# Performance work log

Hardware: AMD Instinct MI355X
Metric: run time of the kernel (lower is better)

The kernel has to match this reference:

```python
import jax, jax.numpy as jnp
import numpy as np


def setup_inputs() -> dict:
    key = jax.random.key(0)
    k1, k2, k3 = jax.random.split(key, 3)
    B, L, D = 2, 8192, 1024
    x = jax.random.normal(k1, (B, L, D), dtype=jnp.float32)
    h = jax.random.normal(k2, (L, D), dtype=jnp.float32)
    bias = jax.random.normal(k3, (D,), dtype=jnp.float32) * 0.02
    return {"x": x, "h": h, "bias": bias}


def reference(x, h, bias):
    # x: (B, L, D), h: (filter_len, D), bias: (D,)
    B, L, D = x.shape
    filter_len = h.shape[0]
    # next power of two >= L + filter_len - 1 (static, from shapes)
    fft_size = 1 << int(L + filter_len - 1).bit_length()
    x_f = jnp.fft.rfft(x, n=fft_size, axis=1)          # (B, fft_size//2+1, D) complex
    h_f = jnp.fft.rfft(h, n=fft_size, axis=0)          # (fft_size//2+1, D) complex
    y = jnp.fft.irfft(x_f * h_f[None, :, :], n=fft_size, axis=1)
    y = y[:, :L, :]                                    # causal-length truncation
    return y + bias
```

## Files before the change

### kernel.cpp

```cpp
#include <hip/hip_runtime.h>

#define D_CH   1024
#define L_SEQ  8192
#define NCH    32
#define W_N    3.8349519697141029e-4f
#define W128A  4.90873852123405e-2f

__device__ __forceinline__ float bf2f(unsigned v){
  union { float f; unsigned u; } x; x.u = v << 16;
  return x.f;
}
__device__ __forceinline__ unsigned packc(float r, float i){
  unsigned u;
  asm("v_cvt_pk_bf16_f32 %0, %1, %2" : "=v"(u) : "v"(r), "v"(i));
  return u;
}
__device__ __forceinline__ float2 upk(unsigned u){
  return make_float2(bf2f(u & 0xffffu), bf2f(u >> 16));
}
__device__ __forceinline__ float4 upk2(uint2 u){
  return make_float4(bf2f(u.x & 0xffffu), bf2f(u.x >> 16),
                     bf2f(u.y & 0xffffu), bf2f(u.y >> 16));
}
__device__ __forceinline__ float4 cmul2(float4 a, float cs, float sn){
  return make_float4(a.x*cs - a.y*sn, a.x*sn + a.y*cs,
                     a.z*cs - a.w*sn, a.z*sn + a.w*cs);
}

__device__ __host__ constexpr int bitrev4(int j){
  return ((j&1)<<3)|((j&2)<<1)|((j&4)>>1)|((j&8)>>3);
}
__device__ __host__ constexpr int bitrev3(int j){
  return ((j&1)<<2)|(j&2)|((j&4)>>2);
}

template<int SGN>
__device__ __forceinline__ void dft16(float2* x){
  const float TC[8] = {1.f, 0.9238795325f, 0.7071067812f, 0.3826834324f,
                       0.f, -0.3826834324f, -0.7071067812f, -0.9238795325f};
  const float TS[8] = {0.f, -0.3826834324f, -0.7071067812f, -0.9238795325f,
                       -1.f, -0.9238795325f, -0.7071067812f, -0.3826834324f};
#pragma unroll
  for (int len = 16; len >= 2; len >>= 1){
    const int half = len >> 1, tstep = 16 / len;
#pragma unroll
    for (int st = 0; st < 16; st += len){
#pragma unroll
      for (int j = 0; j < half; j++){
        const float wr = TC[j*tstep];
        const float wi = (SGN > 0) ? TS[j*tstep] : -TS[j*tstep];
        const int a = st + j, b = a + half;
        const float ur = x[a].x, ui = x[a].y;
        const float vr = x[b].x, vi = x[b].y;
        x[a].x = ur + vr; x[a].y = ui + vi;
        const float dr = ur - vr, di = ui - vi;
        x[b].x = dr*wr - di*wi;
        x[b].y = dr*wi + di*wr;
      }
    }
  }
}

template<int SGN>
__device__ __forceinline__ void dft8(float2* x){
  const float TC[4] = {1.f, 0.7071067812f, 0.f, -0.7071067812f};
  const float TS[4] = {0.f, -0.7071067812f, -1.f, -0.7071067812f};
#pragma unroll
  for (int len = 8; len >= 2; len >>= 1){
    const int half = len >> 1, tstep = 8 / len;
#pragma unroll
    for (int st = 0; st < 8; st += len){
#pragma unroll
      for (int j = 0; j < half; j++){
        const float wr = TC[j*tstep];
        const float wi = (SGN > 0) ? TS[j*tstep] : -TS[j*tstep];
        const int a = st + j, b = a + half;
        const float ur = x[a].x, ui = x[a].y;
        const float vr = x[b].x, vi = x[b].y;
        x[a].x = ur + vr; x[a].y = ui + vi;
        const float dr = ur - vr, di = ui - vi;
        x[b].x = dr*wr - di*wi;
        x[b].y = dr*wi + di*wr;
      }
    }
  }
}

template<int SGN>
__device__ __forceinline__ void dft16v4(float4* x){
  const float TC[8] = {1.f, 0.9238795325f, 0.7071067812f, 0.3826834324f,
                       0.f, -0.3826834324f, -0.7071067812f, -0.9238795325f};
  const float TS[8] = {0.f, -0.3826834324f, -0.7071067812f, -0.9238795325f,
                       -1.f, -0.9238795325f, -0.7071067812f, -0.3826834324f};
#pragma unroll
  for (int len = 16; len >= 2; len >>= 1){
    const int half = len >> 1, tstep = 16 / len;
#pragma unroll
    for (int st = 0; st < 16; st += len){
#pragma unroll
      for (int j = 0; j < half; j++){
        const float wr = TC[j*tstep];
        const float wi = (SGN > 0) ? TS[j*tstep] : -TS[j*tstep];
        const int a = st + j, b = a + half;
        const float4 u = x[a], v = x[b];
        x[a] = make_float4(u.x+v.x, u.y+v.y, u.z+v.z, u.w+v.w);
        const float4 dd = make_float4(u.x-v.x, u.y-v.y, u.z-v.z, u.w-v.w);
        x[b] = make_float4(dd.x*wr - dd.y*wi, dd.x*wi + dd.y*wr,
                           dd.z*wr - dd.w*wi, dd.z*wi + dd.w*wr);
      }
    }
  }
}

template<int SGN>
__device__ __forceinline__ void dft8v4(float4* x){
  const float TC[4] = {1.f, 0.7071067812f, 0.f, -0.7071067812f};
  const float TS[4] = {0.f, -0.7071067812f, -1.f, -0.7071067812f};
#pragma unroll
  for (int len = 8; len >= 2; len >>= 1){
    const int half = len >> 1, tstep = 8 / len;
#pragma unroll
    for (int st = 0; st < 8; st += len){
#pragma unroll
      for (int j = 0; j < half; j++){
        const float wr = TC[j*tstep];
        const float wi = (SGN > 0) ? TS[j*tstep] : -TS[j*tstep];
        const int a = st + j, b = a + half;
        const float4 u = x[a], v = x[b];
        x[a] = make_float4(u.x+v.x, u.y+v.y, u.z+v.z, u.w+v.w);
        const float4 dd = make_float4(u.x-v.x, u.y-v.y, u.z-v.z, u.w-v.w);
        x[b] = make_float4(dd.x*wr - dd.y*wi, dd.x*wi + dd.y*wr,
                           dd.z*wr - dd.w*wi, dd.z*wi + dd.w*wr);
      }
    }
  }
}

__device__ __forceinline__ void build_twF(float2* twF, int tid){
  if (tid < 128){
    const int pp = tid >> 4, kk = tid & 15;
    float sn, cs;
    __sincosf(-W128A * (float)(pp * kk), &sn, &cs);
    twF[tid] = make_float2(cs, sn);
  }
}

template<int SGN>
__device__ __forceinline__ void fft128(float2* v, float2* lds,
                                       const float2* twF, int ch, int p){
  dft16<SGN>(v);
#pragma unroll
  for (int slot = 0; slot < 8; slot++){
    const int r = bitrev3(slot);
    const float2 t = twF[p*16 + 2*r];
    const float cs = t.x;
    const float sn = (SGN > 0) ? t.y : -t.y;
    const float2 a = v[slot];
    lds[(p*8 + r)*NCH + ch] = make_float2(a.x*cs - a.y*sn, a.x*sn + a.y*cs);
  }
  __syncthreads();
  float2 t8[8];
#pragma unroll
  for (int pp = 0; pp < 8; pp++) t8[pp] = lds[(pp*8 + p)*NCH + ch];
  dft8<SGN>(t8);
#pragma unroll
  for (int t = 0; t < 8; t++) v[t] = t8[t];
  __syncthreads();
#pragma unroll
  for (int slot = 8; slot < 16; slot++){
    const int r = bitrev3(slot - 8);
    const float2 t = twF[p*16 + 2*r + 1];
    const float cs = t.x;
    const float sn = (SGN > 0) ? t.y : -t.y;
    const float2 a = v[slot];
    lds[(p*8 + r)*NCH + ch] = make_float2(a.x*cs - a.y*sn, a.x*sn + a.y*cs);
  }
  __syncthreads();
#pragma unroll
  for (int pp = 0; pp < 8; pp++) t8[pp] = lds[(pp*8 + p)*NCH + ch];
  dft8<SGN>(t8);
#pragma unroll
  for (int t = 0; t < 8; t++) v[8 + t] = t8[t];
}

template<int SGN>
__device__ __forceinline__ void fft128v4(float4* v, float4* lds4,
                                         const float2* twF, int ch, int p){
  dft16v4<SGN>(v);
#pragma unroll
  for (int slot = 0; slot < 8; slot++){
    const int r = bitrev3(slot);
    const float2 t = twF[p*16 + 2*r];
    const float cs = t.x;
    const float sn = (SGN > 0) ? t.y : -t.y;
    lds4[(p*8 + r)*32 + ch] = cmul2(v[slot], cs, sn);
  }
  __syncthreads();
  float4 t8[8];
#pragma unroll
  for (int pp = 0; pp < 8; pp++) t8[pp] = lds4[(pp*8 + p)*32 + ch];
  dft8v4<SGN>(t8);
#pragma unroll
  for (int t = 0; t < 8; t++) v[t] = t8[t];
  __syncthreads();
#pragma unroll
  for (int slot = 8; slot < 16; slot++){
    const int r = bitrev3(slot - 8);
    const float2 t = twF[p*16 + 2*r + 1];
    const float cs = t.x;
    const float sn = (SGN > 0) ? t.y : -t.y;
    lds4[(p*8 + r)*32 + ch] = cmul2(v[slot], cs, sn);
  }
  __syncthreads();
#pragma unroll
  for (int pp = 0; pp < 8; pp++) t8[pp] = lds4[(pp*8 + p)*32 + ch];
  dft8v4<SGN>(t8);
#pragma unroll
  for (int t = 0; t < 8; t++) v[8 + t] = t8[t];
}

__global__ __launch_bounds__(256, 4)
void k1_step1(const float* __restrict__ x, const float* __restrict__ h,
              unsigned* __restrict__ Az, unsigned* __restrict__ Ah){
  __shared__ float4 lds4[64*32];
  __shared__ float2 twF[128];
  __shared__ float2 twO[128];
  const int n2 = blockIdx.x, dg = blockIdx.y, mode = blockIdx.z;
  const int tid = threadIdx.x;
  const int ch = tid & 31, p = tid >> 5;
  const int d = dg*64 + 2*ch;

  build_twF(twF, tid);
  if (tid >= 128 && tid < 256){
    const int k1v = tid - 128;
    float sn, cs;
    __sincosf(-W_N * (float)(k1v * n2), &sn, &cs);
    twO[k1v] = make_float2(cs, sn);
  }

  float4 v[16];
  if (mode == 0){
    const float* x0 = x;
    const float* x1 = x + (size_t)L_SEQ * D_CH;
#pragma unroll
    for (int q = 0; q < 8; q++){
      const size_t off = (size_t)(n2 + 128*(p + 8*q)) * D_CH + d;
      const float2 a = *(const float2*)(x0 + off);
      const float2 b = *(const float2*)(x1 + off);
      v[q] = make_float4(a.x, b.x, a.y, b.y);
    }
  } else {
#pragma unroll
    for (int q = 0; q < 8; q++){
      const size_t off = (size_t)(n2 + 128*(p + 8*q)) * D_CH + d;
      const float2 a = *(const float2*)(h + off);
      v[q] = make_float4(a.x, 0.f, a.y, 0.f);
    }
  }
#pragma unroll
  for (int q = 8; q < 16; q++) v[q] = make_float4(0.f, 0.f, 0.f, 0.f);

  __syncthreads();
  fft128v4<1>(v, lds4, twF, ch, p);

  unsigned* __restrict__ A = mode ? Ah : Az;
#pragma unroll
  for (int c = 0; c < 2; c++){
#pragma unroll
    for (int t = 0; t < 8; t++){
      const int k1v = (2*p + c) + 16*bitrev3(t);
      const float2 w = twO[k1v];
      const float4 r = cmul2(v[c*8 + t], w.x, w.y);
      *(uint2*)&A[((size_t)k1v*128 + n2)*D_CH + d] =
        make_uint2(packc(r.x, r.y), packc(r.z, r.w));
    }
  }
}

__global__ __launch_bounds__(256, 4)
void k2_zh(unsigned* __restrict__ Az, const unsigned* __restrict__ Ah){
  __shared__ float2 lds[64*NCH];
  __shared__ float2 twF[128];
  const int k1 = blockIdx.x, dg = blockIdx.y;
  const int tid = threadIdx.x;
  const int ch = tid & (NCH-1), p = tid >> 5;
  const int d = dg*NCH + ch;
  const size_t base = (size_t)k1 * 128 * D_CH + d;

  build_twF(twF, tid);

  unsigned ha[16], za[16];
#pragma unroll
  for (int q = 0; q < 16; q++)
    ha[q] = Ah[base + (size_t)(p + 8*q) * D_CH];
#pragma unroll
  for (int q = 0; q < 16; q++)
    za[q] = Az[base + (size_t)(p + 8*q) * D_CH];

  __syncthreads();

  float2 v[16];
#pragma unroll
  for (int q = 0; q < 16; q++) v[q] = upk(ha[q]);
  fft128<1>(v, lds, twF, ch, p);
  unsigned hs[16];
  const float sc = 1.0f / 16384.0f;
#pragma unroll
  for (int i = 0; i < 16; i++) hs[i] = packc(v[i].x * sc, v[i].y * sc);
  __syncthreads();

#pragma unroll
  for (int q = 0; q < 16; q++) v[q] = upk(za[q]);
  fft128<1>(v, lds, twF, ch, p);

#pragma unroll
  for (int i = 0; i < 16; i++){
    const float2 hv = upk(hs[i]);
    const float zr = v[i].x, zi = v[i].y;
    v[i] = make_float2(zr*hv.x - zi*hv.y, zr*hv.y + zi*hv.x);
  }

  __syncthreads();
  float2 w[8];
#pragma unroll
  for (int c = 0; c < 2; c++)
#pragma unroll
    for (int t = 0; t < 8; t += 2){
      const int k2 = (2*p + c) + 16*bitrev3(t);
      lds[k2*NCH + ch] = v[c*8 + t];
    }
  __syncthreads();
#pragma unroll
  for (int q = 0; q < 8; q++) w[q] = lds[(p + 8*q)*NCH + ch];
  __syncthreads();
#pragma unroll
  for (int c = 0; c < 2; c++)
#pragma unroll
    for (int t = 1; t < 8; t += 2){
      const int k2 = (2*p + c) + 16*bitrev3(t) - 64;
      lds[k2*NCH + ch] = v[c*8 + t];
    }
  __syncthreads();
#pragma unroll
  for (int q = 0; q < 8; q++) v[8 + q] = lds[(p + 8*q)*NCH + ch];
  __syncthreads();
#pragma unroll
  for (int q = 0; q < 8; q++) v[q] = w[q];

  fft128<-1>(v, lds, twF, ch, p);

#pragma unroll
  for (int c = 0; c < 2; c++){
#pragma unroll
    for (int t = 0; t < 8; t++){
      const int m2 = (2*p + c) + 16*bitrev3(t);
      const float2 a = v[c*8 + t];
      Az[base + (size_t)m2 * D_CH] = packc(a.x, a.y);
    }
  }
}

__global__ __launch_bounds__(256, 4)
void k3_inv2(const unsigned* __restrict__ Bz, const float* __restrict__ bias,
             float* __restrict__ out){
  __shared__ float4 lds4[64*32];
  __shared__ float2 twF[128];
  __shared__ float2 twI[128];
  const int m2 = blockIdx.x, dg = blockIdx.y;
  const int tid = threadIdx.x;
  const int ch = tid & 31, p = tid >> 5;
  const int d = dg*64 + 2*ch;
  const float2 bv = *(const float2*)(bias + d);

  build_twF(twF, tid);
  if (tid >= 128 && tid < 256){
    const int k1 = tid - 128;
    float sn, cs;
    __sincosf(W_N * (float)(m2 * k1), &sn, &cs);
    twI[k1] = make_float2(cs, sn);
  }

  uint2 raw[16];
#pragma unroll
  for (int q = 0; q < 16; q++){
    const int k1 = p + 8*q;
    raw[q] = *(const uint2*)&Bz[((size_t)k1*128 + m2) * D_CH + d];
  }

  __syncthreads();

  float4 v[16];
#pragma unroll
  for (int q = 0; q < 16; q++){
    const float2 w = twI[p + 8*q];
    v[q] = cmul2(upk2(raw[q]), w.x, w.y);
  }

  fft128v4<-1>(v, lds4, twF, ch, p);

#pragma unroll
  for (int c = 0; c < 2; c++){
#pragma unroll
    for (int t = 0; t < 8; t += 2){
      const int m1 = (2*p + c) + 16*bitrev3(t);
      const int tseq = m2 + 128*m1;
      const float4 a = v[c*8 + t];
      *(float2*)&out[(size_t)tseq * D_CH + d] =
        make_float2(a.x + bv.x, a.z + bv.y);
      *(float2*)&out[(size_t)(L_SEQ + tseq) * D_CH + d] =
        make_float2(a.y + bv.x, a.w + bv.y);
    }
  }
}

extern "C" void kernel_launch(void* const* d_in, const int* in_sizes, int n_in,
                              void* d_out, int out_size, void* d_ws, size_t ws_size,
                              hipStream_t stream){
  (void)in_sizes; (void)n_in; (void)out_size;
  const float* x    = (const float*)d_in[0];
  const float* h    = (const float*)d_in[1];
  const float* bias = (const float*)d_in[2];
  float* out = (float*)d_out;

  const size_t REGION = (size_t)128 * 128 * D_CH * sizeof(unsigned);
  unsigned *r1, *r2;
  if (ws_size >= 2 * REGION){
    r1 = (unsigned*)d_ws;
    r2 = (unsigned*)((char*)d_ws + REGION);
  } else {
    r1 = (unsigned*)d_out;
    r2 = (unsigned*)d_ws;
  }

  const dim3 blk(256, 1, 1);
  hipLaunchKernelGGL(k1_step1, dim3(128,16,2), blk, 0, stream, x, h, r1, r2);
  hipLaunchKernelGGL(k2_zh,    dim3(128,32,1), blk, 0, stream, r1, r2);
  hipLaunchKernelGGL(k3_inv2,  dim3(128,16,1), blk, 0, stream, r1, bias, out);
}
```

Baseline: 236.7 us.

## Make FFT stages wave-local with double-buffered register prefetch across tiles

Result: slower. 388.9 us (+64.3%).

```diff
diff --git a/kernel.cpp b/kernel.cpp
--- a/kernel.cpp
+++ b/kernel.cpp
@@ -2,7 +2,6 @@
 
 #define D_CH   1024
 #define L_SEQ  8192
-#define NCH    32
 #define W_N    3.8349519697141029e-4f
 #define W128A  4.90873852123405e-2f
 
@@ -27,11 +26,13 @@
                      a.z*cs - a.w*sn, a.z*sn + a.w*cs);
 }
 
-__device__ __host__ constexpr int bitrev4(int j){
-  return ((j&1)<<3)|((j&2)<<1)|((j&4)>>1)|((j&8)>>3);
-}
 __device__ __host__ constexpr int bitrev3(int j){
   return ((j&1)<<2)|(j&2)|((j&4)>>2);
+}
+
+__device__ __forceinline__ void lds_fence(){
+  asm volatile("s_waitcnt lgkmcnt(0)" ::: "memory");
+  __builtin_amdgcn_sched_barrier(0);
 }
 
 template<int SGN>
@@ -113,14 +114,24 @@
 }
 
 template<int SGN>
-__device__ __forceinline__ void dft8v4(float4* x){
-  const float TC[4] = {1.f, 0.7071067812f, 0.f, -0.7071067812f};
-  const float TS[4] = {0.f, -0.7071067812f, -1.f, -0.7071067812f};
+__device__ __forceinline__ void dft16zv4(float4* x){
+  const float TC[8] = {1.f, 0.9238795325f, 0.7071067812f, 0.3826834324f,
+                       0.f, -0.3826834324f, -0.7071067812f, -0.9238795325f};
+  const float TS[8] = {0.f, -0.3826834324f, -0.7071067812f, -0.9238795325f,
+                       -1.f, -0.9238795325f, -0.7071067812f, -0.3826834324f};
+#pragma unroll
+  for (int j = 0; j < 8; j++){
+    const float wr = TC[j];
+    const float wi = (SGN > 0) ? TS[j] : -TS[j];
+    const float4 u = x[j];
+    x[j+8] = make_float4(u.x*wr - u.y*wi, u.x*wi + u.y*wr,
+                         u.z*wr - u.w*wi, u.z*wi + u.w*wr);
+  }
 #pragma unroll
   for (int len = 8; len >= 2; len >>= 1){
-    const int half = len >> 1, tstep = 8 / len;
-#pragma unroll
-    for (int st = 0; st < 8; st += len){
+    const int half = len >> 1, tstep = 16 / len;
+#pragma unroll
+    for (int st = 0; st < 16; st += len){
 #pragma unroll
       for (int j = 0; j < half; j++){
         const float wr = TC[j*tstep];
@@ -136,279 +147,361 @@
   }
 }
 
-__device__ __forceinline__ void build_twF(float2* twF, int tid){
+template<int SGN>
+__device__ __forceinline__ void dft8v4(float4* x){
+  const float TC[4] = {1.f, 0.7071067812f, 0.f, -0.7071067812f};
+  const float TS[4] = {0.f, -0.7071067812f, -1.f, -0.7071067812f};
+#pragma unroll
+  for (int len = 8; len >= 2; len >>= 1){
+    const int half = len >> 1, tstep = 8 / len;
+#pragma unroll
+    for (int st = 0; st < 8; st += len){
+#pragma unroll
+      for (int j = 0; j < half; j++){
+        const float wr = TC[j*tstep];
+        const float wi = (SGN > 0) ? TS[j*tstep] : -TS[j*tstep];
+        const int a = st + j, b = a + half;
+        const float4 u = x[a], v = x[b];
+        x[a] = make_float4(u.x+v.x, u.y+v.y, u.z+v.z, u.w+v.w);
+        const float4 dd = make_float4(u.x-v.x, u.y-v.y, u.z-v.z, u.w-v.w);
+        x[b] = make_float4(dd.x*wr - dd.y*wi, dd.x*wi + dd.y*wr,
+                           dd.z*wr - dd.w*wi, dd.z*wi + dd.w*wr);
+      }
+    }
+  }
+}
+
+template<int SGN, bool ZT>
+__device__ __forceinline__ void fft128w4(float4* v, float4* buf,
+                                         const float2* twF, int c8, int p){
+  lds_fence();
+  if (ZT) dft16zv4<SGN>(v); else dft16v4<SGN>(v);
+#pragma unroll
+  for (int slot = 0; slot < 8; slot++){
+    const int r = bitrev3(slot);
+    const float2 t = twF[p*16 + 2*r];
+    const float cs = t.x, sn = (SGN > 0) ? t.y : -t.y;
+    buf[(p*8 + r)*8 + c8] = cmul2(v[slot], cs, sn);
+  }
+  lds_fence();
+  float4 t8[8];
+#pragma unroll
+  for (int pp = 0; pp < 8; pp++) t8[pp] = buf[(pp*8 + p)*8 + c8];
+  lds_fence();
+  dft8v4<SGN>(t8);
+#pragma unroll
+  for (int t = 0; t < 8; t++) v[t] = t8[t];
+#pragma unroll
+  for (int slot = 8; slot < 16; slot++){
+    const int r = bitrev3(slot - 8);
+    const float2 t = twF[p*16 + 2*r + 1];
+    const float cs = t.x, sn = (SGN > 0) ? t.y : -t.y;
+    buf[(p*8 + r)*8 + c8] = cmul2(v[slot], cs, sn);
+  }
+  lds_fence();
+#pragma unroll
+  for (int pp = 0; pp < 8; pp++) t8[pp] = buf[(pp*8 + p)*8 + c8];
+  dft8v4<SGN>(t8);
+#pragma unroll
+  for (int t = 0; t < 8; t++) v[8 + t] = t8[t];
+}
+
+template<int SGN>
+__device__ __forceinline__ void fft128w2(float2* v, float2* buf,
+                                         const float2* twF, int c8, int p){
+  lds_fence();
+  dft16<SGN>(v);
+#pragma unroll
+  for (int slot = 0; slot < 8; slot++){
+    const int r = bitrev3(slot);
+    const float2 t = twF[p*16 + 2*r];
+    const float cs = t.x, sn = (SGN > 0) ? t.y : -t.y;
+    const float2 a = v[slot];
+    buf[(p*8 + r)*9 + c8] = make_float2(a.x*cs - a.y*sn, a.x*sn + a.y*cs);
+  }
+  lds_fence();
+  float2 t8[8];
+#pragma unroll
+  for (int pp = 0; pp < 8; pp++) t8[pp] = buf[(pp*8 + p)*9 + c8];
+  lds_fence();
+  dft8<SGN>(t8);
+#pragma unroll
+  for (int t = 0; t < 8; t++) v[t] = t8[t];
+#pragma unroll
+  for (int slot = 8; slot < 16; slot++){
+    const int r = bitrev3(slot - 8);
+    const float2 t = twF[p*16 + 2*r + 1];
+    const float cs = t.x, sn = (SGN > 0) ? t.y : -t.y;
+    const float2 a = v[slot];
+    buf[(p*8 + r)*9 + c8] = make_float2(a.x*cs - a.y*sn, a.x*sn + a.y*cs);
+  }
+  lds_fence();
+#pragma unroll
+  for (int pp = 0; pp < 8; pp++) t8[pp] = buf[(pp*8 + p)*9 + c8];
+  dft8<SGN>(t8);
+#pragma unroll
+  for (int t = 0; t < 8; t++) v[8 + t] = t8[t];
+}
+
+__global__ __launch_bounds__(256, 2)
+void k1_step1(const float* __restrict__ x, const float* __restrict__ h,
+              unsigned* __restrict__ Az, unsigned* __restrict__ Ah){
+  __shared__ float4 xch[4][64*8];
+  __shared__ float2 twF[128];
+  __shared__ float2 twO[128];
+  const int n2 = blockIdx.x, dh = blockIdx.y, mode = blockIdx.z;
+  const int tid = threadIdx.x;
+  const int wv = tid >> 6, lane = tid & 63;
+  const int p = lane >> 3, c8 = lane & 7;
+  const float* x1 = x + (size_t)L_SEQ * D_CH;
+  unsigned* __restrict__ A = mode ? Ah : Az;
+  float4* buf = xch[wv];
+
+  float2 a0[8], a1[8], b0[8], b1[8];
+
+  auto loadT = [&](int i, float2 (&r0)[8], float2 (&r1)[8]){
+    const int d = dh*512 + i*64 + wv*16 + c8*2;
+    if (mode == 0){
+#pragma unroll
+      for (int q = 0; q < 8; q++){
+        const size_t off = (size_t)(n2 + 128*(p + 8*q)) * D_CH + d;
+        r0[q] = *(const float2*)(x  + off);
+        r1[q] = *(const float2*)(x1 + off);
+      }
+    } else {
+#pragma unroll
+      for (int q = 0; q < 8; q++){
+        const size_t off = (size_t)(n2 + 128*(p + 8*q)) * D_CH + d;
+        r0[q] = *(const float2*)(h + off);
+      }
+    }
+  };
+
+  auto runT = [&](int i, float2 (&r0)[8], float2 (&r1)[8]){
+    const int d = dh*512 + i*64 + wv*16 + c8*2;
+    float4 v[16];
+    if (mode == 0){
+#pragma unroll
+      for (int q = 0; q < 8; q++)
+        v[q] = make_float4(r0[q].x, r1[q].x, r0[q].y, r1[q].y);
+    } else {
+#pragma unroll
+      for (int q = 0; q < 8; q++)
+        v[q] = make_float4(r0[q].x, 0.f, r0[q].y, 0.f);
+    }
+    fft128w4<1, true>(v, buf, twF, c8, p);
+#pragma unroll
+    for (int c = 0; c < 2; c++)
+#pragma unroll
+      for (int t = 0; t < 8; t++){
+        const int k1v = (2*p + c) + 16*bitrev3(t);
+        if (mode == 1 && k1v > 64) continue;
+        const float2 w = twO[k1v];
+        const float4 r = cmul2(v[c*8 + t], w.x, w.y);
+        *(uint2*)&A[((size_t)k1v*128 + n2)*D_CH + d] =
+          make_uint2(packc(r.x, r.y), packc(r.z, r.w));
+      }
+  };
+
+  loadT(0, a0, a1);
   if (tid < 128){
     const int pp = tid >> 4, kk = tid & 15;
     float sn, cs;
     __sincosf(-W128A * (float)(pp * kk), &sn, &cs);
     twF[tid] = make_float2(cs, sn);
-  }
-}
-
-template<int SGN>
-__device__ __forceinline__ void fft128(float2* v, float2* lds,
-                                       const float2* twF, int ch, int p){
-  dft16<SGN>(v);
-#pragma unroll
-  for (int slot = 0; slot < 8; slot++){
-    const int r = bitrev3(slot);
-    const float2 t = twF[p*16 + 2*r];
-    const float cs = t.x;
-    const float sn = (SGN > 0) ? t.y : -t.y;
-    const float2 a = v[slot];
-    lds[(p*8 + r)*NCH + ch] = make_float2(a.x*cs - a.y*sn, a.x*sn + a.y*cs);
-  }
-  __syncthreads();
-  float2 t8[8];
-#pragma unroll
-  for (int pp = 0; pp < 8; pp++) t8[pp] = lds[(pp*8 + p)*NCH + ch];
-  dft8<SGN>(t8);
-#pragma unroll
-  for (int t = 0; t < 8; t++) v[t] = t8[t];
-  __syncthreads();
-#pragma unroll
-  for (int slot = 8; slot < 16; slot++){
-    const int r = bitrev3(slot - 8);
-    const float2 t = twF[p*16 + 2*r + 1];
-    const float cs = t.x;
-    const float sn = (SGN > 0) ? t.y : -t.y;
-    const float2 a = v[slot];
-    lds[(p*8 + r)*NCH + ch] = make_float2(a.x*cs - a.y*sn, a.x*sn + a.y*cs);
-  }
-  __syncthreads();
-#pragma unroll
-  for (int pp = 0; pp < 8; pp++) t8[pp] = lds[(pp*8 + p)*NCH + ch];
-  dft8<SGN>(t8);
-#pragma unroll
-  for (int t = 0; t < 8; t++) v[8 + t] = t8[t];
-}
-
-template<int SGN>
-__device__ __forceinline__ void fft128v4(float4* v, float4* lds4,
-                                         const float2* twF, int ch, int p){
-  dft16v4<SGN>(v);
-#pragma unroll
-  for (int slot = 0; slot < 8; slot++){
-    const int r = bitrev3(slot);
-    const float2 t = twF[p*16 + 2*r];
-    const float cs = t.x;
-    const float sn = (SGN > 0) ? t.y : -t.y;
-    lds4[(p*8 + r)*32 + ch] = cmul2(v[slot], cs, sn);
-  }
-  __syncthreads();
-  float4 t8[8];
-#pragma unroll
-  for (int pp = 0; pp < 8; pp++) t8[pp] = lds4[(pp*8 + p)*32 + ch];
-  dft8v4<SGN>(t8);
-#pragma unroll
-  for (int t = 0; t < 8; t++) v[t] = t8[t];
-  __syncthreads();
-#pragma unroll
-  for (int slot = 8; slot < 16; slot++){
-    const int r = bitrev3(slot - 8);
-    const float2 t = twF[p*16 + 2*r + 1];
-    const float cs = t.x;
-    const float sn = (SGN > 0) ? t.y : -t.y;
-    lds4[(p*8 + r)*32 + ch] = cmul2(v[slot], cs, sn);
-  }
-  __syncthreads();
-#pragma unroll
-  for (int pp = 0; pp < 8; pp++) t8[pp] = lds4[(pp*8 + p)*32 + ch];
-  dft8v4<SGN>(t8);
-#pragma unroll
-  for (int t = 0; t < 8; t++) v[8 + t] = t8[t];
-}
-
-__global__ __launch_bounds__(256, 4)
-void k1_step1(const float* __restrict__ x, const float* __restrict__ h,
-              unsigned* __restrict__ Az, unsigned* __restrict__ Ah){
-  __shared__ float4 lds4[64*32];
-  __shared__ float2 twF[128];
-  __shared__ float2 twO[128];
-  const int n2 = blockIdx.x, dg = blockIdx.y, mode = blockIdx.z;
-  const int tid = threadIdx.x;
-  const int ch = tid & 31, p = tid >> 5;
-  const int d = dg*64 + 2*ch;
-
-  build_twF(twF, tid);
-  if (tid >= 128 && tid < 256){
+  } else {
     const int k1v = tid - 128;
     float sn, cs;
     __sincosf(-W_N * (float)(k1v * n2), &sn, &cs);
     twO[k1v] = make_float2(cs, sn);
   }
-
-  float4 v[16];
-  if (mode == 0){
-    const float* x0 = x;
-    const float* x1 = x + (size_t)L_SEQ * D_CH;
-#pragma unroll
-    for (int q = 0; q < 8; q++){
-      const size_t off = (size_t)(n2 + 128*(p + 8*q)) * D_CH + d;
-      const float2 a = *(const float2*)(x0 + off);
-      const float2 b = *(const float2*)(x1 + off);
-      v[q] = make_float4(a.x, b.x, a.y, b.y);
-    }
+  __syncthreads();
+
+#pragma unroll
+  for (int i = 0; i < 8; i++){
+    if (i & 1){
+      if (i+1 < 8) loadT(i+1, a0, a1);
+      runT(i, b0, b1);
+    } else {
+      if (i+1 < 8) loadT(i+1, b0, b1);
+      runT(i, a0, a1);
+    }
+  }
+}
+
+__global__ __launch_bounds__(256, 2)
+void k2_zh(unsigned* __restrict__ Az, const unsigned* __restrict__ Ah){
+  __shared__ float2 rbuf[4][128*9];
+  __shared__ float2 twF[128];
+  __shared__ float2 tw1[128];
+  const int k1 = blockIdx.x, dq = blockIdx.y;
+  const int tid = threadIdx.x;
+  const int wv = tid >> 6, lane = tid & 63;
+  const int p = lane >> 3, c8 = lane & 7;
+  const int k1r = (k1 > 64) ? 128 - k1 : k1;
+  float2* buf = rbuf[wv];
+
+  unsigned haA[16], zaA[16], haB[16], zaB[16];
+
+  auto loadT = [&](int i, unsigned (&ha)[16], unsigned (&za)[16]){
+    const int d = dq*256 + i*32 + wv*8 + c8;
+    const size_t bh = (size_t)k1r * 128 * D_CH + d;
+    const size_t bz = (size_t)k1  * 128 * D_CH + d;
+#pragma unroll
+    for (int q = 0; q < 16; q++) ha[q] = Ah[bh + (size_t)(p + 8*q) * D_CH];
+#pragma unroll
+    for (int q = 0; q < 16; q++) za[q] = Az[bz + (size_t)(p + 8*q) * D_CH];
+  };
+
+  auto runT = [&](int i, unsigned (&ha)[16], unsigned (&za)[16]){
+    const int d = dq*256 + i*32 + wv*8 + c8;
+    const size_t bz = (size_t)k1 * 128 * D_CH + d;
+    float2 v[16];
+    if (k1 <= 64){
+#pragma unroll
+      for (int q = 0; q < 16; q++) v[q] = upk(ha[q]);
+    } else {
+#pragma unroll
+      for (int q = 0; q < 16; q++){
+        const float2 a = upk(ha[q]);
+        const float2 t = tw1[p + 8*q];
+        v[q] = make_float2(t.x*a.x + t.y*a.y, t.y*a.x - t.x*a.y);
+      }
+    }
+    fft128w2<1>(v, buf, twF, c8, p);
+    unsigned hs[16];
+    const float sc = 1.0f / 16384.0f;
+#pragma unroll
+    for (int j = 0; j < 16; j++) hs[j] = packc(v[j].x * sc, v[j].y * sc);
+
+#pragma unroll
+    for (int q = 0; q < 16; q++) v[q] = upk(za[q]);
+    fft128w2<1>(v, buf, twF, c8, p);
+
+#pragma unroll
+    for (int j = 0; j < 16; j++){
+      const float2 hv = upk(hs[j]);
+      const float zr = v[j].x, zi = v[j].y;
+      v[j] = make_float2(zr*hv.x - zi*hv.y, zr*hv.y + zi*hv.x);
+    }
+
+    lds_fence();
+#pragma unroll
+    for (int c = 0; c < 2; c++)
+#pragma unroll
+      for (int t = 0; t < 8; t++){
+        const int k2i = (2*p + c) + 16*bitrev3(t);
+        buf[k2i*9 + c8] = v[c*8 + t];
+      }
+    lds_fence();
+#pragma unroll
+    for (int q = 0; q < 16; q++) v[q] = buf[(p + 8*q)*9 + c8];
+
+    fft128w2<-1>(v, buf, twF, c8, p);
+
+#pragma unroll
+    for (int c = 0; c < 2; c++)
+#pragma unroll
+      for (int t = 0; t < 8; t++){
+        const int m2 = (2*p + c) + 16*bitrev3(t);
+        const float2 a = v[c*8 + t];
+        Az[bz + (size_t)m2 * D_CH] = packc(a.x, a.y);
+      }
+  };
+
+  loadT(0, haA, zaA);
+  if (tid < 128){
+    const int pp = tid >> 4, kk = tid & 15;
+    float sn, cs;
+    __sincosf(-W128A * (float)(pp * kk), &sn, &cs);
+    twF[tid] = make_float2(cs, sn);
   } else {
-#pragma unroll
-    for (int q = 0; q < 8; q++){
-      const size_t off = (size_t)(n2 + 128*(p + 8*q)) * D_CH + d;
-      const float2 a = *(const float2*)(h + off);
-      v[q] = make_float4(a.x, 0.f, a.y, 0.f);
-    }
-  }
-#pragma unroll
-  for (int q = 8; q < 16; q++) v[q] = make_float4(0.f, 0.f, 0.f, 0.f);
-
+    const int n = tid - 128;
+    float sn, cs;
+    __sincosf(-W128A * (float)n, &sn, &cs);
+    tw1[n] = make_float2(cs, sn);
+  }
   __syncthreads();
-  fft128v4<1>(v, lds4, twF, ch, p);
-
-  unsigned* __restrict__ A = mode ? Ah : Az;
-#pragma unroll
-  for (int c = 0; c < 2; c++){
-#pragma unroll
-    for (int t = 0; t < 8; t++){
-      const int k1v = (2*p + c) + 16*bitrev3(t);
-      const float2 w = twO[k1v];
-      const float4 r = cmul2(v[c*8 + t], w.x, w.y);
-      *(uint2*)&A[((size_t)k1v*128 + n2)*D_CH + d] =
-        make_uint2(packc(r.x, r.y), packc(r.z, r.w));
-    }
-  }
-}
-
-__global__ __launch_bounds__(256, 4)
-void k2_zh(unsigned* __restrict__ Az, const unsigned* __restrict__ Ah){
-  __shared__ float2 lds[64*NCH];
-  __shared__ float2 twF[128];
-  const int k1 = blockIdx.x, dg = blockIdx.y;
-  const int tid = threadIdx.x;
-  const int ch = tid & (NCH-1), p = tid >> 5;
-  const int d = dg*NCH + ch;
-  const size_t base = (size_t)k1 * 128 * D_CH + d;
-
-  build_twF(twF, tid);
-
-  unsigned ha[16], za[16];
-#pragma unroll
-  for (int q = 0; q < 16; q++)
-    ha[q] = Ah[base + (size_t)(p + 8*q) * D_CH];
-#pragma unroll
-  for (int q = 0; q < 16; q++)
-    za[q] = Az[base + (size_t)(p + 8*q) * D_CH];
-
-  __syncthreads();
-
-  float2 v[16];
-#pragma unroll
-  for (int q = 0; q < 16; q++) v[q] = upk(ha[q]);
-  fft128<1>(v, lds, twF, ch, p);
-  unsigned hs[16];
-  const float sc = 1.0f / 16384.0f;
-#pragma unroll
-  for (int i = 0; i < 16; i++) hs[i] = packc(v[i].x * sc, v[i].y * sc);
-  __syncthreads();
-
-#pragma unroll
-  for (int q = 0; q < 16; q++) v[q] = upk(za[q]);
-  fft128<1>(v, lds, twF, ch, p);
-
-#pragma unroll
-  for (int i = 0; i < 16; i++){
-    const float2 hv = upk(hs[i]);
-    const float zr = v[i].x, zi = v[i].y;
-    v[i] = make_float2(zr*hv.x - zi*hv.y, zr*hv.y + zi*hv.x);
-  }
-
-  __syncthreads();
-  float2 w[8];
-#pragma unroll
-  for (int c = 0; c < 2; c++)
-#pragma unroll
-    for (int t = 0; t < 8; t += 2){
-      const int k2 = (2*p + c) + 16*bitrev3(t);
-      lds[k2*NCH + ch] = v[c*8 + t];
-    }
-  __syncthreads();
-#pragma unroll
-  for (int q = 0; q < 8; q++) w[q] = lds[(p + 8*q)*NCH + ch];
-  __syncthreads();
-#pragma unroll
-  for (int c = 0; c < 2; c++)
-#pragma unroll
-    for (int t = 1; t < 8; t += 2){
-      const int k2 = (2*p + c) + 16*bitrev3(t) - 64;
-      lds[k2*NCH + ch] = v[c*8 + t];
-    }
-  __syncthreads();
-#pragma unroll
-  for (int q = 0; q < 8; q++) v[8 + q] = lds[(p + 8*q)*NCH + ch];
-  __syncthreads();
-#pragma unroll
-  for (int q = 0; q < 8; q++) v[q] = w[q];
-
-  fft128<-1>(v, lds, twF, ch, p);
-
-#pragma unroll
-  for (int c = 0; c < 2; c++){
-#pragma unroll
-    for (int t = 0; t < 8; t++){
-      const int m2 = (2*p + c) + 16*bitrev3(t);
-      const float2 a = v[c*8 + t];
-      Az[base + (size_t)m2 * D_CH] = packc(a.x, a.y);
-    }
-  }
-}
-
-__global__ __launch_bounds__(256, 4)
+
+#pragma unroll
+  for (int i = 0; i < 8; i++){
+    if (i & 1){
+      if (i+1 < 8) loadT(i+1, haA, zaA);
+      runT(i, haB, zaB);
+    } else {
+      if (i+1 < 8) loadT(i+1, haB, zaB);
+      runT(i, haA, zaA);
+    }
+  }
+}
+
+__global__ __launch_bounds__(256, 2)
 void k3_inv2(const unsigned* __restrict__ Bz, const float* __restrict__ bias,
              float* __restrict__ out){
-  __shared__ float4 lds4[64*32];
+  __shared__ float4 xch[4][64*8];
   __shared__ float2 twF[128];
   __shared__ float2 twI[128];
-  const int m2 = blockIdx.x, dg = blockIdx.y;
+  const int m2 = blockIdx.x, dq = blockIdx.y;
   const int tid = threadIdx.x;
-  const int ch = tid & 31, p = tid >> 5;
-  const int d = dg*64 + 2*ch;
-  const float2 bv = *(const float2*)(bias + d);
-
-  build_twF(twF, tid);
-  if (tid >= 128 && tid < 256){
+  const int wv = tid >> 6, lane = tid & 63;
+  const int p = lane >> 3, c8 = lane & 7;
+  float4* buf = xch[wv];
+
+  uint2 ra[16], rb[16];
+
+  auto loadT = [&](int i, uint2 (&r)[16]){
+    const int d = dq*256 + i*64 + wv*16 + c8*2;
+#pragma unroll
+    for (int q = 0; q < 16; q++)
+      r[q] = *(const uint2*)&Bz[((size_t)(p + 8*q)*128 + m2) * D_CH + d];
+  };
+
+  auto runT = [&](int i, uint2 (&r)[16]){
+    const int d = dq*256 + i*64 + wv*16 + c8*2;
+    const float2 bv = *(const float2*)(bias + d);
+    float4 v[16];
+#pragma unroll
+    for (int q = 0; q < 16; q++){
+      const float2 w = twI[p + 8*q];
+      v[q] = cmul2(upk2(r[q]), w.x, w.y);
+    }
+    fft128w4<-1, false>(v, buf, twF, c8, p);
+#pragma unroll
+    for (int c = 0; c < 2; c++)
+#pragma unroll
+      for (int t = 0; t < 8; t += 2){
+        const int m1 = (2*p + c) + 16*bitrev3(t);
+        const int tseq = m2 + 128*m1;
+        const float4 a = v[c*8 + t];
+        *(float2*)&out[(size_t)tseq * D_CH + d] =
+          make_float2(a.x + bv.x, a.z + bv.y);
+        *(float2*)&out[(size_t)(L_SEQ + tseq) * D_CH + d] =
+          make_float2(a.y + bv.x, a.w + bv.y);
+      }
+  };
+
+  loadT(0, ra);
+  if (tid < 128){
+    const int pp = tid >> 4, kk = tid & 15;
+    float sn, cs;
+    __sincosf(-W128A * (float)(pp * kk), &sn, &cs);
+    twF[tid] = make_float2(cs, sn);
+  } else {
     const int k1 = tid - 128;
     float sn, cs;
     __sincosf(W_N * (float)(m2 * k1), &sn, &cs);
     twI[k1] = make_float2(cs, sn);
   }
-
-  uint2 raw[16];
-#pragma unroll
-  for (int q = 0; q < 16; q++){
-    const int k1 = p + 8*q;
-    raw[q] = *(const uint2*)&Bz[((size_t)k1*128 + m2) * D_CH + d];
-  }
-
   __syncthreads();
 
-  float4 v[16];
-#pragma unroll
-  for (int q = 0; q < 16; q++){
-    const float2 w = twI[p + 8*q];
-    v[q] = cmul2(upk2(raw[q]), w.x, w.y);
-  }
-
-  fft128v4<-1>(v, lds4, twF, ch, p);
-
-#pragma unroll
-  for (int c = 0; c < 2; c++){
-#pragma unroll
-    for (int t = 0; t < 8; t += 2){
-      const int m1 = (2*p + c) + 16*bitrev3(t);
-      const int tseq = m2 + 128*m1;
-      const float4 a = v[c*8 + t];
-      *(float2*)&out[(size_t)tseq * D_CH + d] =
-        make_float2(a.x + bv.x, a.z + bv.y);
-      *(float2*)&out[(size_t)(L_SEQ + tseq) * D_CH + d] =
-        make_float2(a.y + bv.x, a.w + bv.y);
+#pragma unroll
+  for (int i = 0; i < 4; i++){
+    if (i & 1){
+      if (i+1 < 4) loadT(i+1, ra);
+      runT(i, rb);
+    } else {
+      if (i+1 < 4) loadT(i+1, rb);
+      runT(i, ra);
     }
   }
 }
@@ -433,7 +526,7 @@
   }
 
   const dim3 blk(256, 1, 1);
-  hipLaunchKernelGGL(k1_step1, dim3(128,16,2), blk, 0, stream, x, h, r1, r2);
-  hipLaunchKernelGGL(k2_zh,    dim3(128,32,1), blk, 0, stream, r1, r2);
-  hipLaunchKernelGGL(k3_inv2,  dim3(128,16,1), blk, 0, stream, r1, bias, out);
-}
+  hipLaunchKernelGGL(k1_step1, dim3(128,2,2), blk, 0, stream, x, h, r1, r2);
+  hipLaunchKernelGGL(k2_zh,    dim3(128,4,1), blk, 0, stream, r1, r2);
+  hipLaunchKernelGGL(k3_inv2,  dim3(128,4,1), blk, 0, stream, r1, bias, out);
+}
```
